# Performance work log

Measured on AMD Instinct MI355X. Metric: run time of the kernel, lower is better.

Reference implementation:

```python
import jax, jax.numpy as jnp
from jax import lax
import numpy as np

K_LIST = [2, 4, 8]

def setup_inputs() -> dict:
    key = jax.random.key(0)
    k1, k2 = jax.random.split(key)
    B_, C, H, Wd = 8, 256, 128, 128
    x = jax.random.normal(k1, (B_, C, H, Wd), dtype=jnp.float32)
    # conv weights init ~ N(0, 1e-6) per the module's 'zero' init, bias zero
    W = jax.random.normal(k2, (len(K_LIST), 1, C, 3, 3), dtype=jnp.float32) * 1e-6
    Bb = jnp.zeros((len(K_LIST), 1), dtype=jnp.float32)
    return {"x": x, "W": W, "B": Bb}


def _band_grid(h, w):
    # signed max of (fftfreq_h, rfftfreq_w) coords, matching torch code
    fh = jnp.fft.fftfreq(h).astype(jnp.float32)          # [h]
    fw = jnp.fft.rfftfreq(w).astype(jnp.float32)         # [w//2+1]
    return jnp.maximum(fh[:, None], fw[None, :])         # [h, w//2+1]


def reference(x, W, B):
    b, c, h, w = x.shape
    x_dtype = x.dtype
    x32 = x.astype(jnp.float32)
    x_fft = jnp.fft.rfft2(x32, norm='ortho')             # [b,c,h,w//2+1] complex
    grid = _band_grid(h, w)
    pre_x = x32
    out = jnp.zeros_like(x32)
    for idx, freq in enumerate(K_LIST):
        mask = (grid < 0.5 / freq).astype(jnp.float32)   # [h, w//2+1]
        low = jnp.fft.irfft2(x_fft * mask, s=(h, w), norm='ortho')
        high = pre_x - low
        pre_x = low
        # Conv2d(in=256, out=1, k=3, pad=1) on att_feat=x
        fwgt = lax.conv_general_dilated(
            x32, W[idx], window_strides=(1, 1), padding='SAME',
            dimension_numbers=('NCHW', 'OIHW', 'NCHW'))
        fwgt = fwgt + B[idx][None, :, None, None]        # [b,1,h,w]
        gate = jax.nn.sigmoid(fwgt) * 2.0
        out = out + gate * high                          # broadcast over channels
    out = out + pre_x                                    # residual low-frequency part
    return out.astype(x_dtype)
```

## Files before the change

### kernel.cpp

```cpp
#include <hip/hip_runtime.h>


#define NPIX 16384
#define NCHN 256

typedef __attribute__((ext_vector_type(8))) short bf16x8;
typedef __attribute__((ext_vector_type(4))) float f32x4;

__device__ __align__(16) short g_f[64][128];
__device__ __align__(16) short g_h[192][256];
__device__ __align__(16) short g_e[3][256][192];
__device__ __align__(16) short g_p[3][128][64];

static __device__ __forceinline__ short f2bf(float f) {
  unsigned u = __float_as_uint(f);
  unsigned r = (u + 0x7fffu + ((u >> 16) & 1u)) >> 16;
  return (short)r;
}
static __device__ __forceinline__ float bf2f(short s) {
  return __uint_as_float(((unsigned)(unsigned short)s) << 16);
}
static __device__ __forceinline__ f32x4 mfma16(bf16x8 a, bf16x8 b, f32x4 c) {
  return __builtin_amdgcn_mfma_f32_16x16x32_bf16(a, b, c, 0, 0, 0);
}

__global__ __launch_bounds__(256) void const_init_kernel() {
  int idx = blockIdx.x * 256 + threadIdx.x;
  const float C = 6.2831853071795864769f / 128.f;
  if (idx < 8192) {
    int n = idx >> 7, q = idx & 127;
    int j = n & 31;
    float ang = C * (float)((j * q) & 127);
    float v = (n < 32) ? cosf(ang) : -sinf(ang);
    reinterpret_cast<short*>(g_f)[idx] = f2bf(v);
  } else if (idx < 57344) {
    int e = idx - 8192;
    int d = e >> 8, kk = e & 255;
    int r = (d < 96) ? d : d - 96;
    int ifr = (r < 32) ? r : r + 32;
    float ang = C * (float)((ifr * (kk & 127)) & 127);
    float cv = cosf(ang) * (1.f / 128.f), sv = sinf(ang) * (1.f / 128.f);
    float v = (d < 96) ? ((kk < 128) ? cv : sv) : ((kk < 128) ? -sv : cv);
    reinterpret_cast<short*>(g_h)[e] = f2bf(v);
  } else if (idx < 204800) {
    int e = idx - 57344;
    int k = e / 49152; int e2 = e % 49152;
    int mm = e2 / 192, kk = e2 % 192;
    int nk = 32 >> k;
    int r = (kk < 96) ? kk : kk - 96;
    bool allow = (r < nk) || (r >= 32);
    int ifr = (r < 32) ? r : r + 32;
    float ang = C * (float)((ifr * (mm & 127)) & 127);
    float cv = cosf(ang), sv = sinf(ang);
    float v = (mm < 128) ? ((kk < 96) ? cv : -sv) : ((kk < 96) ? sv : cv);
    reinterpret_cast<short*>(g_e)[e] = f2bf(allow ? v : 0.f);
  } else {
    int e = idx - 204800;
    int k = e / 8192; int e2 = e % 8192;
    int n = e2 >> 6, jj = e2 & 63;
    int nk = 32 >> k;
    int j = jj & 31;
    bool valid = (j < nk) && (jj < 32 || j > 0);
    float wj = (j == 0) ? (1.f / 128.f) : (2.f / 128.f);
    float ang = C * (float)((j * n) & 127);
    float v = (jj < 32) ? (wj * cosf(ang)) : (-wj * sinf(ang));
    reinterpret_cast<short*>(g_p)[e] = f2bf(valid ? v : 0.f);
  }
}

__global__ __launch_bounds__(256) void gates_partial_kernel(
    const float* __restrict__ x, const float* __restrict__ Wg,
    float* __restrict__ partial) {
  int bid = blockIdx.x;
  int b = bid & 7;
  int tile = (bid >> 3) & 63;
  int cs = bid >> 9;
  int m = ((tile >> 3) << 4) + (threadIdx.x >> 4);
  int n = ((tile & 7) << 4) + (threadIdx.x & 15);
  float a0 = 0.f, a1 = 0.f, a2 = 0.f;
  const float* xb = x + (size_t)b * NCHN * NPIX;
  for (int c = cs * 64; c < cs * 64 + 64; ++c) {
    const float* xc = xb + (size_t)c * NPIX;
    const float* wc = Wg + c * 9;
    #pragma unroll
    for (int dh = -1; dh <= 1; ++dh) {
      int gm = m + dh;
      bool vm = (unsigned)gm < 128u;
      #pragma unroll
      for (int dw = -1; dw <= 1; ++dw) {
        int gn = n + dw;
        float xv = (vm && (unsigned)gn < 128u) ? xc[gm * 128 + gn] : 0.f;
        int tap = (dh + 1) * 3 + (dw + 1);
        a0 = fmaf(xv, wc[tap], a0);
        a1 = fmaf(xv, wc[2304 + tap], a1);
        a2 = fmaf(xv, wc[4608 + tap], a2);
      }
    }
  }
  int pix = m * 128 + n;
  float* pp = partial + (size_t)(cs * 8 + b) * 3 * NPIX;
  pp[pix]            = a0;
  pp[NPIX + pix]     = a1;
  pp[2 * NPIX + pix] = a2;
}

__global__ __launch_bounds__(256) void gates_combine_kernel(
    const float* __restrict__ partial, const float* __restrict__ Bg,
    short* __restrict__ dcoef) {
  int bid = blockIdx.x;
  int b = bid & 7;
  int px = (bid >> 3) * 256 + threadIdx.x;
  float a0 = Bg[0], a1 = Bg[1], a2 = Bg[2];
  #pragma unroll
  for (int cs = 0; cs < 4; ++cs) {
    const float* pp = partial + (size_t)(cs * 8 + b) * 3 * NPIX;
    a0 += pp[px];
    a1 += pp[NPIX + px];
    a2 += pp[2 * NPIX + px];
  }
  float g1 = 2.f / (1.f + expf(-a0));
  float g2 = 2.f / (1.f + expf(-a1));
  float g3 = 2.f / (1.f + expf(-a2));
  int pix = b * NPIX + px;
  dcoef[pix]          = f2bf(g1 - 1.f);
  dcoef[131072 + pix] = f2bf(g2 - g1);
  dcoef[262144 + pix] = f2bf(g3 - g2);
  dcoef[393216 + pix] = f2bf(1.f - g3);
}

__global__ __launch_bounds__(256) void gates_kernel(
    const float* __restrict__ x, const float* __restrict__ Wg,
    const float* __restrict__ Bg, short* __restrict__ dcoef) {
  int blk = blockIdx.x;
  int b = blk >> 6;
  int tile = blk & 63;
  int m = ((tile >> 3) << 4) + (threadIdx.x >> 4);
  int n = ((tile & 7) << 4) + (threadIdx.x & 15);
  float a0 = 0.f, a1 = 0.f, a2 = 0.f;
  const float* xb = x + (size_t)b * NCHN * NPIX;
  for (int c = 0; c < NCHN; ++c) {
    const float* xc = xb + (size_t)c * NPIX;
    const float* wc = Wg + c * 9;
    #pragma unroll
    for (int dh = -1; dh <= 1; ++dh) {
      int gm = m + dh;
      bool vm = (unsigned)gm < 128u;
      #pragma unroll
      for (int dw = -1; dw <= 1; ++dw) {
        int gn = n + dw;
        float xv = (vm && (unsigned)gn < 128u) ? xc[gm * 128 + gn] : 0.f;
        int tap = (dh + 1) * 3 + (dw + 1);
        a0 = fmaf(xv, wc[tap], a0);
        a1 = fmaf(xv, wc[2304 + tap], a1);
        a2 = fmaf(xv, wc[4608 + tap], a2);
      }
    }
  }
  a0 += Bg[0]; a1 += Bg[1]; a2 += Bg[2];
  float g1 = 2.f / (1.f + expf(-a0));
  float g2 = 2.f / (1.f + expf(-a1));
  float g3 = 2.f / (1.f + expf(-a2));
  int pix = b * NPIX + m * 128 + n;
  dcoef[pix]          = f2bf(g1 - 1.f);
  dcoef[131072 + pix] = f2bf(g2 - g1);
  dcoef[262144 + pix] = f2bf(g3 - g2);
  dcoef[393216 + pix] = f2bf(1.f - g3);
}

__global__ __launch_bounds__(512, 2) void fbm_kernel(
    const float* __restrict__ x, const short* __restrict__ dcoef,
    float* __restrict__ out) {
  __shared__ __align__(16) short Xs[16384];
  __shared__ __align__(16) short WVs[8192];
  __shared__ __align__(16) short Ds2[6144];
  __shared__ __align__(16) short dls[3][16384];
  char* XsB = reinterpret_cast<char*>(Xs);
  char* PlaneB = XsB;
  char* WsB = reinterpret_cast<char*>(WVs);
  char* DsB = reinterpret_cast<char*>(Ds2);

  int t = threadIdx.x;
  int bid = blockIdx.x;
  int b = bid >> 5;
  int cg = bid & 31;
  size_t img0 = ((size_t)b << 8) + ((size_t)cg << 3);
  int lane = t & 63, w = t >> 6;
  int l15 = lane & 15, l4 = lane >> 4;
  const f32x4 zero = {0.f, 0.f, 0.f, 0.f};

  {
    bf16x8* dst = reinterpret_cast<bf16x8*>(dls);
    for (int i = t; i < 6144; i += 512) {
      int p = i >> 11, o = i & 2047;
      dst[i] = reinterpret_cast<const bf16x8*>(
          dcoef + (size_t)(p + 1) * 131072 + ((size_t)b << 14))[o];
    }
  }
  const short4* d0p = reinterpret_cast<const short4*>(dcoef + ((size_t)b << 14));

  f32x4 xbuf[8];
  {
    const f32x4* xv4 = reinterpret_cast<const f32x4*>(x + img0 * NPIX);
    #pragma unroll
    for (int i = 0; i < 8; ++i)
      xbuf[i] = __builtin_nontemporal_load(&xv4[t + i * 512]);
  }

  for (int c = 0; c < 8; ++c) {
    f32x4 oaccC[8];
    #pragma unroll
    for (int i = 0; i < 8; ++i) {
      int f = t + i * 512;
      f32x4 xv = xbuf[i];
      short4 dv = d0p[f];
      f32x4 dvf = {bf2f(dv.x), bf2f(dv.y), bf2f(dv.z), bf2f(dv.w)};
      oaccC[i] = xv + dvf * xv;
      int row = f >> 5;
      int byte = row * 256 + (((f & 31) * 8) ^ ((row & 7) << 4));
      short4 s;
      s.x = f2bf(xv[0]); s.y = f2bf(xv[1]); s.z = f2bf(xv[2]); s.w = f2bf(xv[3]);
      *reinterpret_cast<short4*>(XsB + byte) = s;
    }
    __syncthreads();

    if (c < 7) {
      const f32x4* xn = reinterpret_cast<const f32x4*>(x + (img0 + c + 1) * NPIX);
      #pragma unroll
      for (int i = 0; i < 8; ++i)
        xbuf[i] = __builtin_nontemporal_load(&xn[t + i * 512]);
    }

    {
      int Ntile = w & 3, Mq = w >> 2;
      int n = Ntile * 16 + l15;
      f32x4 acc[4] = {zero, zero, zero, zero};
      #pragma unroll
      for (int ks = 0; ks < 4; ++ks) {
        int koff = ks * 32 + l4 * 8;
        bf16x8 bf = *reinterpret_cast<const bf16x8*>(&g_f[n][koff]);
        #pragma unroll
        for (int mt = 0; mt < 4; ++mt) {
          int p = (Mq * 4 + mt) * 16 + l15;
          bf16x8 a = *reinterpret_cast<const bf16x8*>(
              XsB + p * 256 + ((koff * 2) ^ ((p & 7) << 4)));
          acc[mt] = mfma16(a, bf, acc[mt]);
        }
      }
      #pragma unroll
      for (int mt = 0; mt < 4; ++mt) {
        int p0 = (Mq * 4 + mt) * 16 + l4 * 4;
        short4 s;
        s.x = f2bf(acc[mt][0]); s.y = f2bf(acc[mt][1]);
        s.z = f2bf(acc[mt][2]); s.w = f2bf(acc[mt][3]);
        *reinterpret_cast<short4*>(WsB + n * 256 + ((p0 * 2) ^ ((n & 7) << 4))) = s;
      }
    }
    __syncthreads();

    {
      int Ntile = w & 1, Mt3 = w >> 1;
      int n = Ntile * 16 + l15;
      f32x4 acc[3] = {zero, zero, zero};
      #pragma unroll
      for (int ks = 0; ks < 8; ++ks) {
        int koff = ks * 32 + l4 * 8;
        int wrow = n + ((ks >= 4) ? 32 : 0);
        bf16x8 bb = *reinterpret_cast<const bf16x8*>(
            WsB + wrow * 256 + (((koff & 127) * 2) ^ ((wrow & 7) << 4)));
        #pragma unroll
        for (int mt = 0; mt < 3; ++mt) {
          int d = (Mt3 * 3 + mt) * 16 + l15;
          bf16x8 aa = *reinterpret_cast<const bf16x8*>(&g_h[d][koff]);
          acc[mt] = mfma16(aa, bb, acc[mt]);
        }
      }
      #pragma unroll
      for (int mt = 0; mt < 3; ++mt) {
        int d0 = (Mt3 * 3 + mt) * 16 + l4 * 4;
        short4 s;
        s.x = f2bf(acc[mt][0]); s.y = f2bf(acc[mt][1]);
        s.z = f2bf(acc[mt][2]); s.w = f2bf(acc[mt][3]);
        *reinterpret_cast<short4*>(DsB + n * 384 + ((d0 * 2) ^ ((n & 7) << 4))) = s;
      }
    }
    __syncthreads();

    int Mg3 = w >> 2, Ng3 = w & 3;
    for (int k = 0; k < 3; ++k) {
      {
        f32x4 acc[2][2] = {{zero, zero}, {zero, zero}};
        #pragma unroll
        for (int ks = 0; ks < 6; ++ks) {
          int koff = ks * 32 + l4 * 8;
          bf16x8 b0 = *reinterpret_cast<const bf16x8*>(
              DsB + l15 * 384 + ((koff * 2) ^ ((l15 & 7) << 4)));
          int j1 = 16 + l15;
          bf16x8 b1 = *reinterpret_cast<const bf16x8*>(
              DsB + j1 * 384 + ((koff * 2) ^ ((j1 & 7) << 4)));
          #pragma unroll
          for (int mi = 0; mi < 2; ++mi) {
            int mstk = (2 * w + mi) * 16 + l15;
            bf16x8 aa = *reinterpret_cast<const bf16x8*>(&g_e[k][mstk][koff]);
            acc[mi][0] = mfma16(aa, b0, acc[mi][0]);
            acc[mi][1] = mfma16(aa, b1, acc[mi][1]);
          }
        }
        #pragma unroll
        for (int mi = 0; mi < 2; ++mi) {
          #pragma unroll
          for (int ni = 0; ni < 2; ++ni) {
            int j = ni * 16 + l15;
            #pragma unroll
            for (int r = 0; r < 4; ++r) {
              int mstk = (2 * w + mi) * 16 + l4 * 4 + r;
              int m = mstk & 127;
              int jst = ((mstk >> 7) << 5) + j;
              *reinterpret_cast<short*>(WsB + m * 128 + ((jst * 2) ^ ((m & 7) << 4))) =
                  f2bf(acc[mi][ni][r]);
            }
          }
        }
      }
      __syncthreads();
      {
        f32x4 acc[4][2] = {{zero, zero}, {zero, zero}, {zero, zero}, {zero, zero}};
        #pragma unroll
        for (int ks = 0; ks < 2; ++ks) {
          int koff = ks * 32 + l4 * 8;
          bf16x8 bfr[2];
          #pragma unroll
          for (int nt = 0; nt < 2; ++nt) {
            int nout = (Ng3 * 2 + nt) * 16 + l15;
            bfr[nt] = *reinterpret_cast<const bf16x8*>(&g_p[k][nout][koff]);
          }
          #pragma unroll
          for (int mt = 0; mt < 4; ++mt) {
            int m = (Mg3 * 4 + mt) * 16 + l15;
            bf16x8 aa = *reinterpret_cast<const bf16x8*>(
                WsB + m * 128 + ((koff * 2) ^ ((m & 7) << 4)));
            acc[mt][0] = mfma16(aa, bfr[0], acc[mt][0]);
            acc[mt][1] = mfma16(aa, bfr[1], acc[mt][1]);
          }
        }
        #pragma unroll
        for (int mt = 0; mt < 4; ++mt) {
          #pragma unroll
          for (int nt = 0; nt < 2; ++nt) {
            int col = (Ng3 * 2 + nt) * 16 + l15;
            #pragma unroll
            for (int r = 0; r < 4; ++r) {
              int row = (Mg3 * 4 + mt) * 16 + l4 * 4 + r;
              int byte = row * 256 + ((col ^ ((row & 7) << 2)) << 1);
              *reinterpret_cast<short*>(PlaneB + byte) = f2bf(acc[mt][nt][r]);
            }
          }
        }
      }
      __syncthreads();
      {
        const short4* dk = reinterpret_cast<const short4*>(dls[k]);
        #pragma unroll
        for (int i = 0; i < 8; ++i) {
          int f = t + i * 512;
          int row = f >> 5;
          int col = (f & 31) * 4;
          int byte = row * 256 + ((col ^ ((row & 7) << 2)) << 1);
          short4 s = *reinterpret_cast<const short4*>(PlaneB + byte);
          short4 dv = dk[f];
          oaccC[i][0] = fmaf(bf2f(dv.x), bf2f(s.x), oaccC[i][0]);
          oaccC[i][1] = fmaf(bf2f(dv.y), bf2f(s.y), oaccC[i][1]);
          oaccC[i][2] = fmaf(bf2f(dv.z), bf2f(s.z), oaccC[i][2]);
          oaccC[i][3] = fmaf(bf2f(dv.w), bf2f(s.w), oaccC[i][3]);
        }
      }
      __syncthreads();
    }

    f32x4* og4 = reinterpret_cast<f32x4*>(out + (img0 + c) * NPIX);
    #pragma unroll
    for (int i = 0; i < 8; ++i) og4[t + i * 512] = oaccC[i];
  }
}

extern "C" void kernel_launch(void* const* d_in, const int* in_sizes, int n_in,
                              void* d_out, int out_size, void* d_ws, size_t ws_size,
                              hipStream_t stream) {
  const float* x  = (const float*)d_in[0];
  const float* Wg = (const float*)d_in[1];
  const float* Bg = (const float*)d_in[2];
  float* out  = (float*)d_out;
  short* dcoef = (short*)d_ws;
  float* partial = (float*)((char*)d_ws + (1u << 20));
  const_init_kernel<<<896, 256, 0, stream>>>();
  if (ws_size >= (size_t)(8u << 20)) {
    gates_partial_kernel<<<2048, 256, 0, stream>>>(x, Wg, partial);
    gates_combine_kernel<<<512, 256, 0, stream>>>(partial, Bg, dcoef);
  } else {
    gates_kernel<<<512, 256, 0, stream>>>(x, Wg, Bg, dcoef);
  }
  fbm_kernel<<<256, 512, 0, stream>>>(x, dcoef, out);
}
```

Before: 306.6 us.

## Double fbm_kernel block to 1024 threads and repartition MFMA tiles per wave

Result: slower. 463.7 us (+51.2%).

```diff
diff --git a/kernel.cpp b/kernel.cpp
--- a/kernel.cpp
+++ b/kernel.cpp
@@ -167,7 +167,7 @@
   dcoef[393216 + pix] = f2bf(1.f - g3);
 }
 
-__global__ __launch_bounds__(512, 2) void fbm_kernel(
+__global__ __launch_bounds__(1024, 4) void fbm_kernel(
     const float* __restrict__ x, const short* __restrict__ dcoef,
     float* __restrict__ out) {
   __shared__ __align__(16) short Xs[16384];
@@ -190,7 +190,7 @@
 
   {
     bf16x8* dst = reinterpret_cast<bf16x8*>(dls);
-    for (int i = t; i < 6144; i += 512) {
+    for (int i = t; i < 6144; i += 1024) {
       int p = i >> 11, o = i & 2047;
       dst[i] = reinterpret_cast<const bf16x8*>(
           dcoef + (size_t)(p + 1) * 131072 + ((size_t)b << 14))[o];
@@ -198,19 +198,19 @@
   }
   const short4* d0p = reinterpret_cast<const short4*>(dcoef + ((size_t)b << 14));
 
-  f32x4 xbuf[8];
+  f32x4 xbuf[4];
   {
     const f32x4* xv4 = reinterpret_cast<const f32x4*>(x + img0 * NPIX);
     #pragma unroll
-    for (int i = 0; i < 8; ++i)
-      xbuf[i] = __builtin_nontemporal_load(&xv4[t + i * 512]);
+    for (int i = 0; i < 4; ++i)
+      xbuf[i] = __builtin_nontemporal_load(&xv4[t + i * 1024]);
   }
 
   for (int c = 0; c < 8; ++c) {
-    f32x4 oaccC[8];
-    #pragma unroll
-    for (int i = 0; i < 8; ++i) {
-      int f = t + i * 512;
+    f32x4 oaccC[4];
+    #pragma unroll
+    for (int i = 0; i < 4; ++i) {
+      int f = t + i * 1024;
       f32x4 xv = xbuf[i];
       short4 dv = d0p[f];
       f32x4 dvf = {bf2f(dv.x), bf2f(dv.y), bf2f(dv.z), bf2f(dv.w)};
@@ -226,29 +226,29 @@
     if (c < 7) {
       const f32x4* xn = reinterpret_cast<const f32x4*>(x + (img0 + c + 1) * NPIX);
       #pragma unroll
-      for (int i = 0; i < 8; ++i)
-        xbuf[i] = __builtin_nontemporal_load(&xn[t + i * 512]);
+      for (int i = 0; i < 4; ++i)
+        xbuf[i] = __builtin_nontemporal_load(&xn[t + i * 1024]);
     }
 
     {
-      int Ntile = w & 3, Mq = w >> 2;
-      int n = Ntile * 16 + l15;
-      f32x4 acc[4] = {zero, zero, zero, zero};
+      int Nt = w & 3, Mq = w >> 2;
+      int n = Nt * 16 + l15;
+      f32x4 acc[2] = {zero, zero};
       #pragma unroll
       for (int ks = 0; ks < 4; ++ks) {
         int koff = ks * 32 + l4 * 8;
         bf16x8 bf = *reinterpret_cast<const bf16x8*>(&g_f[n][koff]);
         #pragma unroll
-        for (int mt = 0; mt < 4; ++mt) {
-          int p = (Mq * 4 + mt) * 16 + l15;
+        for (int mt = 0; mt < 2; ++mt) {
+          int p = (Mq * 2 + mt) * 16 + l15;
           bf16x8 a = *reinterpret_cast<const bf16x8*>(
               XsB + p * 256 + ((koff * 2) ^ ((p & 7) << 4)));
           acc[mt] = mfma16(a, bf, acc[mt]);
         }
       }
       #pragma unroll
-      for (int mt = 0; mt < 4; ++mt) {
-        int p0 = (Mq * 4 + mt) * 16 + l4 * 4;
+      for (int mt = 0; mt < 2; ++mt) {
+        int p0 = (Mq * 2 + mt) * 16 + l4 * 4;
         short4 s;
         s.x = f2bf(acc[mt][0]); s.y = f2bf(acc[mt][1]);
         s.z = f2bf(acc[mt][2]); s.w = f2bf(acc[mt][3]);
@@ -257,38 +257,32 @@
     }
     __syncthreads();
 
-    {
-      int Ntile = w & 1, Mt3 = w >> 1;
-      int n = Ntile * 16 + l15;
-      f32x4 acc[3] = {zero, zero, zero};
+    for (int jj = w; jj < 24; jj += 16) {
+      int Nt = jj & 1, Mt = jj >> 1;
+      int n = Nt * 16 + l15;
+      f32x4 acc = zero;
       #pragma unroll
       for (int ks = 0; ks < 8; ++ks) {
         int koff = ks * 32 + l4 * 8;
         int wrow = n + ((ks >= 4) ? 32 : 0);
         bf16x8 bb = *reinterpret_cast<const bf16x8*>(
             WsB + wrow * 256 + (((koff & 127) * 2) ^ ((wrow & 7) << 4)));
-        #pragma unroll
-        for (int mt = 0; mt < 3; ++mt) {
-          int d = (Mt3 * 3 + mt) * 16 + l15;
-          bf16x8 aa = *reinterpret_cast<const bf16x8*>(&g_h[d][koff]);
-          acc[mt] = mfma16(aa, bb, acc[mt]);
-        }
-      }
-      #pragma unroll
-      for (int mt = 0; mt < 3; ++mt) {
-        int d0 = (Mt3 * 3 + mt) * 16 + l4 * 4;
-        short4 s;
-        s.x = f2bf(acc[mt][0]); s.y = f2bf(acc[mt][1]);
-        s.z = f2bf(acc[mt][2]); s.w = f2bf(acc[mt][3]);
-        *reinterpret_cast<short4*>(DsB + n * 384 + ((d0 * 2) ^ ((n & 7) << 4))) = s;
-      }
+        int d = Mt * 16 + l15;
+        bf16x8 aa = *reinterpret_cast<const bf16x8*>(&g_h[d][koff]);
+        acc = mfma16(aa, bb, acc);
+      }
+      int d0 = Mt * 16 + l4 * 4;
+      short4 s;
+      s.x = f2bf(acc[0]); s.y = f2bf(acc[1]);
+      s.z = f2bf(acc[2]); s.w = f2bf(acc[3]);
+      *reinterpret_cast<short4*>(DsB + n * 384 + ((d0 * 2) ^ ((n & 7) << 4))) = s;
     }
     __syncthreads();
 
-    int Mg3 = w >> 2, Ng3 = w & 3;
+    int Mg = w >> 2, Ng = w & 3;
     for (int k = 0; k < 3; ++k) {
       {
-        f32x4 acc[2][2] = {{zero, zero}, {zero, zero}};
+        f32x4 acc[2] = {zero, zero};
         #pragma unroll
         for (int ks = 0; ks < 6; ++ks) {
           int koff = ks * 32 + l4 * 8;
@@ -297,45 +291,39 @@
           int j1 = 16 + l15;
           bf16x8 b1 = *reinterpret_cast<const bf16x8*>(
               DsB + j1 * 384 + ((koff * 2) ^ ((j1 & 7) << 4)));
+          int mstk = w * 16 + l15;
+          bf16x8 aa = *reinterpret_cast<const bf16x8*>(&g_e[k][mstk][koff]);
+          acc[0] = mfma16(aa, b0, acc[0]);
+          acc[1] = mfma16(aa, b1, acc[1]);
+        }
+        #pragma unroll
+        for (int ni = 0; ni < 2; ++ni) {
+          int j = ni * 16 + l15;
           #pragma unroll
-          for (int mi = 0; mi < 2; ++mi) {
-            int mstk = (2 * w + mi) * 16 + l15;
-            bf16x8 aa = *reinterpret_cast<const bf16x8*>(&g_e[k][mstk][koff]);
-            acc[mi][0] = mfma16(aa, b0, acc[mi][0]);
-            acc[mi][1] = mfma16(aa, b1, acc[mi][1]);
-          }
-        }
-        #pragma unroll
-        for (int mi = 0; mi < 2; ++mi) {
-          #pragma unroll
-          for (int ni = 0; ni < 2; ++ni) {
-            int j = ni * 16 + l15;
-            #pragma unroll
-            for (int r = 0; r < 4; ++r) {
-              int mstk = (2 * w + mi) * 16 + l4 * 4 + r;
-              int m = mstk & 127;
-              int jst = ((mstk >> 7) << 5) + j;
-              *reinterpret_cast<short*>(WsB + m * 128 + ((jst * 2) ^ ((m & 7) << 4))) =
-                  f2bf(acc[mi][ni][r]);
-            }
+          for (int r = 0; r < 4; ++r) {
+            int mstk = w * 16 + l4 * 4 + r;
+            int m = mstk & 127;
+            int jst = ((mstk >> 7) << 5) + j;
+            *reinterpret_cast<short*>(WsB + m * 128 + ((jst * 2) ^ ((m & 7) << 4))) =
+                f2bf(acc[ni][r]);
           }
         }
       }
       __syncthreads();
       {
-        f32x4 acc[4][2] = {{zero, zero}, {zero, zero}, {zero, zero}, {zero, zero}};
+        f32x4 acc[2][2] = {{zero, zero}, {zero, zero}};
         #pragma unroll
         for (int ks = 0; ks < 2; ++ks) {
           int koff = ks * 32 + l4 * 8;
           bf16x8 bfr[2];
           #pragma unroll
           for (int nt = 0; nt < 2; ++nt) {
-            int nout = (Ng3 * 2 + nt) * 16 + l15;
+            int nout = (Ng * 2 + nt) * 16 + l15;
             bfr[nt] = *reinterpret_cast<const bf16x8*>(&g_p[k][nout][koff]);
           }
           #pragma unroll
-          for (int mt = 0; mt < 4; ++mt) {
-            int m = (Mg3 * 4 + mt) * 16 + l15;
+          for (int mt = 0; mt < 2; ++mt) {
+            int m = (Mg * 2 + mt) * 16 + l15;
             bf16x8 aa = *reinterpret_cast<const bf16x8*>(
                 WsB + m * 128 + ((koff * 2) ^ ((m & 7) << 4)));
             acc[mt][0] = mfma16(aa, bfr[0], acc[mt][0]);
@@ -343,13 +331,13 @@
           }
         }
         #pragma unroll
-        for (int mt = 0; mt < 4; ++mt) {
+        for (int mt = 0; mt < 2; ++mt) {
           #pragma unroll
           for (int nt = 0; nt < 2; ++nt) {
-            int col = (Ng3 * 2 + nt) * 16 + l15;
+            int col = (Ng * 2 + nt) * 16 + l15;
             #pragma unroll
             for (int r = 0; r < 4; ++r) {
-              int row = (Mg3 * 4 + mt) * 16 + l4 * 4 + r;
+              int row = (Mg * 2 + mt) * 16 + l4 * 4 + r;
               int byte = row * 256 + ((col ^ ((row & 7) << 2)) << 1);
               *reinterpret_cast<short*>(PlaneB + byte) = f2bf(acc[mt][nt][r]);
             }
@@ -360,8 +348,8 @@
       {
         const short4* dk = reinterpret_cast<const short4*>(dls[k]);
         #pragma unroll
-        for (int i = 0; i < 8; ++i) {
-          int f = t + i * 512;
+        for (int i = 0; i < 4; ++i) {
+          int f = t + i * 1024;
           int row = f >> 5;
           int col = (f & 31) * 4;
           int byte = row * 256 + ((col ^ ((row & 7) << 2)) << 1);
@@ -378,7 +366,7 @@
 
     f32x4* og4 = reinterpret_cast<f32x4*>(out + (img0 + c) * NPIX);
     #pragma unroll
-    for (int i = 0; i < 8; ++i) og4[t + i * 512] = oaccC[i];
+    for (int i = 0; i < 4; ++i) og4[t + i * 1024] = oaccC[i];
   }
 }
 
@@ -398,5 +386,5 @@
   } else {
     gates_kernel<<<512, 256, 0, stream>>>(x, Wg, Bg, dcoef);
   }
-  fbm_kernel<<<256, 512, 0, stream>>>(x, dcoef, out);
-}
+  fbm_kernel<<<256, 1024, 0, stream>>>(x, dcoef, out);
+}
```
